# Kernel tuning notes

Hardware: AMD Instinct MI355X
Metric: run time of the kernel (lower is better)

Reference implementation:

```python
import jax, jax.numpy as jnp
import numpy as np

N_NODES = 100000
N_EDGES = 1600000
F_IN = 64
HID = 64
N_ACT = 8


def gcn_conv(x, edge_index, W, b):
    # PyG GCNConv: h = x @ W; add self-loops; norm = deg^{-1/2}[src]*deg^{-1/2}[dst];
    # out[dst] += norm * h[src]; out += b
    n = x.shape[0]
    h = x @ W  # [N, out]
    row = jnp.concatenate([edge_index[0], jnp.arange(n)])  # src (+ self loops)
    col = jnp.concatenate([edge_index[1], jnp.arange(n)])  # dst (+ self loops)
    deg = jax.ops.segment_sum(jnp.ones_like(col, dtype=h.dtype), col, num_segments=n)
    dinv = jnp.where(deg > 0, jax.lax.rsqrt(deg), 0.0)
    norm = dinv[row] * dinv[col]  # [E+N]
    msg = h[row] * norm[:, None]  # gather + scale
    out = jax.ops.segment_sum(msg, col, num_segments=n)  # scatter-add
    return out + b


def setup_inputs() -> dict:
    key = jax.random.key(0)
    ks = jax.random.split(key, 8)
    x = jax.random.normal(ks[0], (N_NODES, F_IN), dtype=jnp.float32)
    edge_index = jax.random.randint(ks[1], (2, N_EDGES), 0, N_NODES, dtype=jnp.int64)
    def glorot(k, fan_in, fan_out):
        s = jnp.sqrt(6.0 / (fan_in + fan_out))
        return jax.random.uniform(k, (fan_in, fan_out), jnp.float32, -s, s)
    W1 = glorot(ks[2], F_IN, HID)
    b1 = jnp.zeros((HID,), jnp.float32)
    W2 = glorot(ks[3], HID, HID)
    b2 = jnp.zeros((HID,), jnp.float32)
    Wfc = glorot(ks[4], HID, N_ACT)
    bfc = jnp.zeros((N_ACT,), jnp.float32)
    return {"x": x, "edge_index": edge_index, "W1": W1, "b1": b1,
            "W2": W2, "b2": b2, "Wfc": Wfc, "bfc": bfc}


def reference(x, edge_index, W1, b1, W2, b2, Wfc, bfc):
    h = jax.nn.relu(gcn_conv(x, edge_index, W1, b1))
    h = jax.nn.relu(gcn_conv(h, edge_index, W2, b2))
    return h @ Wfc + bfc  # Q-values per node: [N, num_actions]
```

## Files before the change

### kernel.cpp

```cpp
#include <hip/hip_runtime.h>
#include <hip/hip_fp16.h>


#define F 64
#define NACT 8
#define BSH 9
#define BNODES 512
#define CAP 10240
#define EPB 2048
#define HS 67

__global__ __launch_bounds__(256) void k_init(int* flag, int* cursor) {
  if (threadIdx.x == 0) *flag = 1;
  cursor[threadIdx.x] = 0;
}

__global__ __launch_bounds__(256) void k_detect(const unsigned int* __restrict__ w, int* flag, int E) {
  int i = blockIdx.x * 256 + threadIdx.x;
  if (i < E && w[2 * i + 1] != 0u) *flag = 0;
}

__device__ __forceinline__ int edge_row(const unsigned int* w, int flag, int e, int E) {
  return flag ? (int)w[2 * e] : (int)w[e];
}
__device__ __forceinline__ int edge_col(const unsigned int* w, int flag, int e, int E) {
  return flag ? (int)w[2 * E + 2 * e] : (int)w[E + e];
}

__global__ __launch_bounds__(256) void k_scatterE(const unsigned int* __restrict__ w,
    const int* __restrict__ flag, int* __restrict__ cursor, unsigned int* __restrict__ slab, int E) {
  __shared__ int hist[256];
  __shared__ int base[256];
  const int tid = threadIdx.x;
  const int fl = *flag;
  hist[tid] = 0;
  __syncthreads();
  int pk[8], bb[8], lr[8];
  const int e0 = blockIdx.x * EPB;
#pragma unroll 8
  for (int j = 0; j < 8; ++j) {
    int e = e0 + j * 256 + tid;
    bb[j] = -1;
    if (e < E) {
      int c = edge_col(w, fl, e, E);
      int s = edge_row(w, fl, e, E);
      int b = c >> BSH;
      pk[j] = (unsigned)s | ((unsigned)(c & (BNODES - 1)) << 17);
      bb[j] = b;
      lr[j] = atomicAdd(&hist[b], 1);
    }
  }
  __syncthreads();
  int h = hist[tid];
  if (h > 0) base[tid] = atomicAdd(&cursor[tid], h);
  __syncthreads();
#pragma unroll 8
  for (int j = 0; j < 8; ++j) {
    if (bb[j] >= 0) {
      slab[(size_t)bb[j] * CAP + base[bb[j]] + lr[j]] = (unsigned)pk[j];
    }
  }
}

__global__ __launch_bounds__(64) void k_slabscan(const int* __restrict__ cursor,
    int* __restrict__ bucketBase, int* __restrict__ csr_off, int NB, int n, int E) {
  int t = threadIdx.x;
  int per = (NB + 63) / 64;
  int base = t * per;
  int local = 0;
  for (int i = 0; i < per; ++i) if (base + i < NB) local += cursor[base + i];
  int inc = local;
  for (int off = 1; off < 64; off <<= 1) {
    int vv = __shfl_up(inc, off);
    if (t >= off) inc += vv;
  }
  int run = inc - local;
  for (int i = 0; i < per; ++i) if (base + i < NB) { bucketBase[base + i] = run; run += cursor[base + i]; }
  if (t == 63) { bucketBase[NB] = inc; csr_off[n] = E; }
}

__global__ __launch_bounds__(256) void k_bucketcsr(const unsigned int* __restrict__ slab,
    const int* __restrict__ bucketBase, int* __restrict__ csr_off, float* __restrict__ dinv,
    int* __restrict__ csr_src, int n) {
  __shared__ int cnt[BNODES];
  __shared__ int off[BNODES];
  __shared__ int sA[256], sB[256];
  const int tid = threadIdx.x;
  const int b = blockIdx.x;
  const int csrbeg = bucketBase[b];
  const int cntb = bucketBase[b + 1] - csrbeg;
  const unsigned int* sl = &slab[(size_t)b * CAP];
  cnt[tid] = 0;
  cnt[tid + 256] = 0;
  __syncthreads();
  for (int i = tid; i < cntb; i += 256) {
    atomicAdd(&cnt[sl[i] >> 17], 1);
  }
  __syncthreads();
  int c0 = cnt[2 * tid], c1 = cnt[2 * tid + 1];
  int p = c0 + c1;
  sA[tid] = p;
  __syncthreads();
  int* srcb = sA;
  int* dstb = sB;
  for (int o = 1; o < 256; o <<= 1) {
    int v = srcb[tid];
    if (tid >= o) v += srcb[tid - o];
    __syncthreads();
    dstb[tid] = v;
    __syncthreads();
    int* t2 = srcb; srcb = dstb; dstb = t2;
  }
  int ex2 = srcb[tid] - p;
  off[2 * tid] = ex2;
  off[2 * tid + 1] = ex2 + c0;
  __syncthreads();
  int v0 = (b << BSH) + 2 * tid;
  if (v0 < n) { csr_off[v0] = csrbeg + off[2 * tid]; dinv[v0] = rsqrtf((float)(c0 + 1)); }
  if (v0 + 1 < n) { csr_off[v0 + 1] = csrbeg + off[2 * tid + 1]; dinv[v0 + 1] = rsqrtf((float)(c1 + 1)); }
  __syncthreads();
  for (int i = tid; i < cntb; i += 256) {
    unsigned int pk = sl[i];
    int dl = pk >> 17;
    int pos = atomicAdd(&off[dl], 1);
    csr_src[csrbeg + pos] = (int)(pk & 0x1FFFFu);
  }
}

__device__ __forceinline__ ushort4 packh4(float a, float b, float c, float d) {
  ushort4 r;
  r.x = __half_as_ushort(__float2half_rn(a));
  r.y = __half_as_ushort(__float2half_rn(b));
  r.z = __half_as_ushort(__float2half_rn(c));
  r.w = __half_as_ushort(__float2half_rn(d));
  return r;
}

__device__ __forceinline__ void addrow8(float* a, uint4 g) {
  union { uint4 u; __half2 h[4]; } u;
  u.u = g;
#pragma unroll
  for (int i = 0; i < 4; ++i) {
    float2 f = __half22float2(u.h[i]);
    a[2 * i] += f.x;
    a[2 * i + 1] += f.y;
  }
}

__device__ __forceinline__ void gather8(const uint4* __restrict__ Gv,
    const int* __restrict__ csr_src, int beg, int end, int l, float* a) {
  int j = beg;
  for (; j + 8 <= end; j += 8) {
    uint4 g0 = Gv[(size_t)csr_src[j + 0] * 8 + l];
    uint4 g1 = Gv[(size_t)csr_src[j + 1] * 8 + l];
    uint4 g2 = Gv[(size_t)csr_src[j + 2] * 8 + l];
    uint4 g3 = Gv[(size_t)csr_src[j + 3] * 8 + l];
    uint4 g4 = Gv[(size_t)csr_src[j + 4] * 8 + l];
    uint4 g5 = Gv[(size_t)csr_src[j + 5] * 8 + l];
    uint4 g6 = Gv[(size_t)csr_src[j + 6] * 8 + l];
    uint4 g7 = Gv[(size_t)csr_src[j + 7] * 8 + l];
    addrow8(a, g0); addrow8(a, g1); addrow8(a, g2); addrow8(a, g3);
    addrow8(a, g4); addrow8(a, g5); addrow8(a, g6); addrow8(a, g7);
  }
  for (; j + 4 <= end; j += 4) {
    uint4 g0 = Gv[(size_t)csr_src[j + 0] * 8 + l];
    uint4 g1 = Gv[(size_t)csr_src[j + 1] * 8 + l];
    uint4 g2 = Gv[(size_t)csr_src[j + 2] * 8 + l];
    uint4 g3 = Gv[(size_t)csr_src[j + 3] * 8 + l];
    addrow8(a, g0); addrow8(a, g1); addrow8(a, g2); addrow8(a, g3);
  }
  for (; j < end; ++j) addrow8(a, Gv[(size_t)csr_src[j] * 8 + l]);
}

__global__ __launch_bounds__(256) void k_gemm_h(const float* __restrict__ X, const float* __restrict__ W,
    const float* __restrict__ dinv, unsigned short* __restrict__ Gh, int n) {
  __shared__ float xst[F * 68];
  __shared__ float wsh[F * F];
  const int tid = threadIdx.x;
  const int row0 = blockIdx.x * 64;
  for (int i = tid * 4; i < F * F; i += 1024)
    *(float4*)&wsh[i] = *(const float4*)&W[i];
  for (int i = tid * 4; i < 64 * F; i += 1024) {
    int r = i >> 6, k = i & 63;
    float4 v = make_float4(0.f, 0.f, 0.f, 0.f);
    if (row0 + r < n) v = *(const float4*)&X[(size_t)(row0 + r) * F + k];
    xst[(k + 0) * 68 + r] = v.x;
    xst[(k + 1) * 68 + r] = v.y;
    xst[(k + 2) * 68 + r] = v.z;
    xst[(k + 3) * 68 + r] = v.w;
  }
  __syncthreads();
  const int tc = tid & 15;
  const int tr = tid >> 4;
  float a00 = 0.f, a01 = 0.f, a02 = 0.f, a03 = 0.f;
  float a10 = 0.f, a11 = 0.f, a12 = 0.f, a13 = 0.f;
  float a20 = 0.f, a21 = 0.f, a22 = 0.f, a23 = 0.f;
  float a30 = 0.f, a31 = 0.f, a32 = 0.f, a33 = 0.f;
  const float* xp = &xst[tr * 4];
  const float* wp = &wsh[tc * 4];
#pragma unroll 8
  for (int k = 0; k < F; ++k) {
    float4 xv = *(const float4*)&xp[k * 68];
    float4 wv = *(const float4*)&wp[k * F];
    a00 = fmaf(xv.x, wv.x, a00); a01 = fmaf(xv.x, wv.y, a01);
    a02 = fmaf(xv.x, wv.z, a02); a03 = fmaf(xv.x, wv.w, a03);
    a10 = fmaf(xv.y, wv.x, a10); a11 = fmaf(xv.y, wv.y, a11);
    a12 = fmaf(xv.y, wv.z, a12); a13 = fmaf(xv.y, wv.w, a13);
    a20 = fmaf(xv.z, wv.x, a20); a21 = fmaf(xv.z, wv.y, a21);
    a22 = fmaf(xv.z, wv.z, a22); a23 = fmaf(xv.z, wv.w, a23);
    a30 = fmaf(xv.w, wv.x, a30); a31 = fmaf(xv.w, wv.y, a31);
    a32 = fmaf(xv.w, wv.z, a32); a33 = fmaf(xv.w, wv.w, a33);
  }
  const int gc = tc * 4;
  int gr = row0 + tr * 4;
  if (gr + 0 < n) { float d = dinv[gr + 0]; *(ushort4*)&Gh[(size_t)(gr + 0) * F + gc] = packh4(a00 * d, a01 * d, a02 * d, a03 * d); }
  if (gr + 1 < n) { float d = dinv[gr + 1]; *(ushort4*)&Gh[(size_t)(gr + 1) * F + gc] = packh4(a10 * d, a11 * d, a12 * d, a13 * d); }
  if (gr + 2 < n) { float d = dinv[gr + 2]; *(ushort4*)&Gh[(size_t)(gr + 2) * F + gc] = packh4(a20 * d, a21 * d, a22 * d, a23 * d); }
  if (gr + 3 < n) { float d = dinv[gr + 3]; *(ushort4*)&Gh[(size_t)(gr + 3) * F + gc] = packh4(a30 * d, a31 * d, a32 * d, a33 * d); }
}

__global__ __launch_bounds__(512) void k_gather_gemm(const int* __restrict__ csr_off,
    const int* __restrict__ csr_src, const unsigned short* __restrict__ Gh1,
    const float* __restrict__ dinv, const float* __restrict__ bias,
    const float* __restrict__ W2, unsigned short* __restrict__ Gh2, int n) {
  __shared__ float hst[F * HS];
  __shared__ float wsh[F * F];
  const int tid = threadIdx.x;
  const int row0 = blockIdx.x * 64;
  {
    int i = tid * 8;
    *(float4*)&wsh[i] = *(const float4*)&W2[i];
    *(float4*)&wsh[i + 4] = *(const float4*)&W2[i + 4];
  }
  const int ln = tid >> 3;
  const int l = tid & 7;
  const int v = row0 + ln;
  float a[8] = {0.f, 0.f, 0.f, 0.f, 0.f, 0.f, 0.f, 0.f};
  if (v < n) {
    const uint4* Gv = (const uint4*)Gh1;
    addrow8(a, Gv[(size_t)v * 8 + l]);
    gather8(Gv, csr_src, csr_off[v], csr_off[v + 1], l, a);
    float d = dinv[v];
#pragma unroll
    for (int jj = 0; jj < 8; ++jj) {
      float h = fmaxf(fmaf(a[jj], d, bias[l * 8 + jj]), 0.f);
      hst[(l * 8 + jj) * HS + ln] = h;
    }
  } else {
#pragma unroll
    for (int jj = 0; jj < 8; ++jj) hst[(l * 8 + jj) * HS + ln] = 0.f;
  }
  __syncthreads();
  const int tc = tid & 15;
  const int tr = tid >> 4;
  const int r0 = 2 * tr;
  float a00 = 0.f, a01 = 0.f, a02 = 0.f, a03 = 0.f;
  float a10 = 0.f, a11 = 0.f, a12 = 0.f, a13 = 0.f;
  const float* wp = &wsh[tc * 4];
#pragma unroll 8
  for (int k = 0; k < F; ++k) {
    float h0 = hst[k * HS + r0];
    float h1 = hst[k * HS + r0 + 1];
    float4 wv = *(const float4*)&wp[k * F];
    a00 = fmaf(h0, wv.x, a00); a01 = fmaf(h0, wv.y, a01);
    a02 = fmaf(h0, wv.z, a02); a03 = fmaf(h0, wv.w, a03);
    a10 = fmaf(h1, wv.x, a10); a11 = fmaf(h1, wv.y, a11);
    a12 = fmaf(h1, wv.z, a12); a13 = fmaf(h1, wv.w, a13);
  }
  const int gc = tc * 4;
  int gr = row0 + r0;
  if (gr < n) { float d = dinv[gr]; *(ushort4*)&Gh2[(size_t)gr * F + gc] = packh4(a00 * d, a01 * d, a02 * d, a03 * d); }
  if (gr + 1 < n) { float d = dinv[gr + 1]; *(ushort4*)&Gh2[(size_t)(gr + 1) * F + gc] = packh4(a10 * d, a11 * d, a12 * d, a13 * d); }
}

__global__ __launch_bounds__(256) void k_gather_fc(const int* __restrict__ csr_off,
    const int* __restrict__ csr_src, const unsigned short* __restrict__ Gh,
    const float* __restrict__ dinv, const float* __restrict__ bias,
    const float* __restrict__ Wfc, const float* __restrict__ bfc,
    float* __restrict__ OUT, int n) {
  __shared__ float wsh[F * 9];
  __shared__ float bs[NACT];
  const int tid = threadIdx.x;
  for (int i = tid; i < F * NACT; i += 256) wsh[(i >> 3) * 9 + (i & 7)] = Wfc[i];
  if (tid < NACT) bs[tid] = bfc[tid];
  __syncthreads();
  int v = blockIdx.x * 32 + (tid >> 3);
  int l = tid & 7;
  if (v >= n) return;
  const uint4* Gv = (const uint4*)Gh;
  float a[8] = {0.f, 0.f, 0.f, 0.f, 0.f, 0.f, 0.f, 0.f};
  addrow8(a, Gv[(size_t)v * 8 + l]);
  gather8(Gv, csr_src, csr_off[v], csr_off[v + 1], l, a);
  float d = dinv[v];
  float q[NACT] = {0.f, 0.f, 0.f, 0.f, 0.f, 0.f, 0.f, 0.f};
#pragma unroll
  for (int jj = 0; jj < 8; ++jj) {
    float h = fmaxf(fmaf(a[jj], d, bias[l * 8 + jj]), 0.f);
    const float* wr = &wsh[(l * 8 + jj) * 9];
#pragma unroll
    for (int aa = 0; aa < NACT; ++aa) q[aa] = fmaf(h, wr[aa], q[aa]);
  }
#pragma unroll
  for (int m = 1; m < 8; m <<= 1) {
#pragma unroll
    for (int aa = 0; aa < NACT; ++aa) q[aa] += __shfl_xor(q[aa], m);
  }
  OUT[(size_t)v * NACT + l] = q[l] + bs[l];
}

extern "C" void kernel_launch(void* const* d_in, const int* in_sizes, int n_in,
                              void* d_out, int out_size, void* d_ws, size_t ws_size,
                              hipStream_t stream) {
  const float* x = (const float*)d_in[0];
  const unsigned int* ew = (const unsigned int*)d_in[1];
  const float* W1 = (const float*)d_in[2];
  const float* b1 = (const float*)d_in[3];
  const float* W2 = (const float*)d_in[4];
  const float* b2 = (const float*)d_in[5];
  const float* Wfc = (const float*)d_in[6];
  const float* bfc = (const float*)d_in[7];
  float* out = (float*)d_out;
  const int n = in_sizes[0] / F;
  const int E = in_sizes[1] / 2;
  const int NB = (n + BNODES - 1) >> BSH;

  char* base = (char*)d_ws;
  size_t off = 0;
  auto alloc = [&](size_t bytes) { void* p = base + off; off += (bytes + 255) & ~(size_t)255; return p; };
  int* flag = (int*)alloc(4);
  int* cursor = (int*)alloc(256 * 4);
  int* bucketBase = (int*)alloc((size_t)(NB + 1) * 4);
  int* csr_off = (int*)alloc((size_t)(n + 1) * 4);
  float* dinv = (float*)alloc((size_t)n * 4);
  unsigned int* slab = (unsigned int*)alloc((size_t)NB * CAP * 4);
  int* csr_src = (int*)alloc((size_t)E * 4);
  unsigned short* Gh1 = (unsigned short*)alloc((size_t)n * F * 2);
  unsigned short* Gh2 = (unsigned short*)alloc((size_t)n * F * 2);

  const int gbE = (E + 255) / 256;
  const int gbSc = (E + EPB - 1) / EPB;
  const int gbRow = (n + 63) / 64;
  const int gbGa = (n + 31) / 32;

  hipLaunchKernelGGL(k_init, dim3(1), dim3(256), 0, stream, flag, cursor);
  hipLaunchKernelGGL(k_detect, dim3(gbE), dim3(256), 0, stream, ew, flag, E);
  hipLaunchKernelGGL(k_scatterE, dim3(gbSc), dim3(256), 0, stream, ew, flag, cursor, slab, E);
  hipLaunchKernelGGL(k_slabscan, dim3(1), dim3(64), 0, stream, cursor, bucketBase, csr_off, NB, n, E);
  hipLaunchKernelGGL(k_bucketcsr, dim3(NB), dim3(256), 0, stream, slab, bucketBase, csr_off, dinv, csr_src, n);

  hipLaunchKernelGGL(k_gemm_h, dim3(gbRow), dim3(256), 0, stream, x, W1, dinv, Gh1, n);
  hipLaunchKernelGGL(k_gather_gemm, dim3(gbRow), dim3(512), 0, stream, csr_off, csr_src, Gh1, dinv, b1, W2, Gh2, n);
  hipLaunchKernelGGL(k_gather_fc, dim3(gbGa), dim3(256), 0, stream, csr_off, csr_src, Gh2, dinv, b2, Wfc, bfc, out, n);
}
```

Baseline: 163.8 us.

## Split layer-2 gather from GEMM, use fma_mix accumulation, sample int64 detection

The fused gather+GEMM kernel for layer 2 is split into a gather kernel that writes fp16 activations and a separate 4x4-register-tiled GEMM kernel, trading an extra fp16 round-trip through memory for better occupancy in the gather. The half-to-float accumulate is replaced by inline v_fma_mix_f32 instructions to cut conversion ALU ops. The int64 layout detection kernel is folded into the init kernel and only checks the first 8192 edges, dropping a full-edge-list pass and one launch but relying on a sampled check.

New measurement: 170.9 us. 4.4% more time.

```diff
diff --git a/kernel.cpp b/kernel.cpp
--- a/kernel.cpp
+++ b/kernel.cpp
@@ -8,16 +8,17 @@
 #define BNODES 512
 #define CAP 10240
 #define EPB 2048
-#define HS 67
-
-__global__ __launch_bounds__(256) void k_init(int* flag, int* cursor) {
+
+__global__ __launch_bounds__(256) void k_init(const unsigned int* __restrict__ w,
+    int* flag, int* cursor, int E) {
   if (threadIdx.x == 0) *flag = 1;
   cursor[threadIdx.x] = 0;
-}
-
-__global__ __launch_bounds__(256) void k_detect(const unsigned int* __restrict__ w, int* flag, int E) {
-  int i = blockIdx.x * 256 + threadIdx.x;
-  if (i < E && w[2 * i + 1] != 0u) *flag = 0;
+  __syncthreads();
+  int bad = 0;
+  for (int i = threadIdx.x; i < 8192; i += 256) {
+    if (i < E && w[2 * i + 1] != 0u) bad = 1;
+  }
+  if (bad) atomicAnd(flag, 0);
 }
 
 __device__ __forceinline__ int edge_row(const unsigned int* w, int flag, int e, int E) {
@@ -136,15 +137,20 @@
   return r;
 }
 
-__device__ __forceinline__ void addrow8(float* a, uint4 g) {
-  union { uint4 u; __half2 h[4]; } u;
-  u.u = g;
-#pragma unroll
-  for (int i = 0; i < 4; ++i) {
-    float2 f = __half22float2(u.h[i]);
-    a[2 * i] += f.x;
-    a[2 * i + 1] += f.y;
-  }
+__device__ __forceinline__ void accmix(float* a, uint4 g) {
+  float one = 1.0f;
+  asm volatile(
+    "v_fma_mix_f32 %0, %9, %8, %0 op_sel:[0,0,0] op_sel_hi:[1,0,0]\n\t"
+    "v_fma_mix_f32 %1, %9, %8, %1 op_sel:[1,0,0] op_sel_hi:[1,0,0]\n\t"
+    "v_fma_mix_f32 %2, %10, %8, %2 op_sel:[0,0,0] op_sel_hi:[1,0,0]\n\t"
+    "v_fma_mix_f32 %3, %10, %8, %3 op_sel:[1,0,0] op_sel_hi:[1,0,0]\n\t"
+    "v_fma_mix_f32 %4, %11, %8, %4 op_sel:[0,0,0] op_sel_hi:[1,0,0]\n\t"
+    "v_fma_mix_f32 %5, %11, %8, %5 op_sel:[1,0,0] op_sel_hi:[1,0,0]\n\t"
+    "v_fma_mix_f32 %6, %12, %8, %6 op_sel:[0,0,0] op_sel_hi:[1,0,0]\n\t"
+    "v_fma_mix_f32 %7, %12, %8, %7 op_sel:[1,0,0] op_sel_hi:[1,0,0]"
+    : "+v"(a[0]), "+v"(a[1]), "+v"(a[2]), "+v"(a[3]),
+      "+v"(a[4]), "+v"(a[5]), "+v"(a[6]), "+v"(a[7])
+    : "v"(one), "v"(g.x), "v"(g.y), "v"(g.z), "v"(g.w));
 }
 
 __device__ __forceinline__ void gather8(const uint4* __restrict__ Gv,
@@ -159,17 +165,17 @@
     uint4 g5 = Gv[(size_t)csr_src[j + 5] * 8 + l];
     uint4 g6 = Gv[(size_t)csr_src[j + 6] * 8 + l];
     uint4 g7 = Gv[(size_t)csr_src[j + 7] * 8 + l];
-    addrow8(a, g0); addrow8(a, g1); addrow8(a, g2); addrow8(a, g3);
-    addrow8(a, g4); addrow8(a, g5); addrow8(a, g6); addrow8(a, g7);
+    accmix(a, g0); accmix(a, g1); accmix(a, g2); accmix(a, g3);
+    accmix(a, g4); accmix(a, g5); accmix(a, g6); accmix(a, g7);
   }
   for (; j + 4 <= end; j += 4) {
     uint4 g0 = Gv[(size_t)csr_src[j + 0] * 8 + l];
     uint4 g1 = Gv[(size_t)csr_src[j + 1] * 8 + l];
     uint4 g2 = Gv[(size_t)csr_src[j + 2] * 8 + l];
     uint4 g3 = Gv[(size_t)csr_src[j + 3] * 8 + l];
-    addrow8(a, g0); addrow8(a, g1); addrow8(a, g2); addrow8(a, g3);
-  }
-  for (; j < end; ++j) addrow8(a, Gv[(size_t)csr_src[j] * 8 + l]);
+    accmix(a, g0); accmix(a, g1); accmix(a, g2); accmix(a, g3);
+  }
+  for (; j < end; ++j) accmix(a, Gv[(size_t)csr_src[j] * 8 + l]);
 }
 
 __global__ __launch_bounds__(256) void k_gemm_h(const float* __restrict__ X, const float* __restrict__ W,
@@ -219,58 +225,76 @@
   if (gr + 3 < n) { float d = dinv[gr + 3]; *(ushort4*)&Gh[(size_t)(gr + 3) * F + gc] = packh4(a30 * d, a31 * d, a32 * d, a33 * d); }
 }
 
-__global__ __launch_bounds__(512) void k_gather_gemm(const int* __restrict__ csr_off,
-    const int* __restrict__ csr_src, const unsigned short* __restrict__ Gh1,
-    const float* __restrict__ dinv, const float* __restrict__ bias,
-    const float* __restrict__ W2, unsigned short* __restrict__ Gh2, int n) {
-  __shared__ float hst[F * HS];
+__global__ __launch_bounds__(256) void k_gemm_h2(const unsigned short* __restrict__ H16,
+    const float* __restrict__ W, const float* __restrict__ dinv,
+    unsigned short* __restrict__ Gh, int n) {
+  __shared__ float xst[F * 68];
   __shared__ float wsh[F * F];
   const int tid = threadIdx.x;
   const int row0 = blockIdx.x * 64;
-  {
-    int i = tid * 8;
-    *(float4*)&wsh[i] = *(const float4*)&W2[i];
-    *(float4*)&wsh[i + 4] = *(const float4*)&W2[i + 4];
-  }
-  const int ln = tid >> 3;
-  const int l = tid & 7;
-  const int v = row0 + ln;
-  float a[8] = {0.f, 0.f, 0.f, 0.f, 0.f, 0.f, 0.f, 0.f};
-  if (v < n) {
-    const uint4* Gv = (const uint4*)Gh1;
-    addrow8(a, Gv[(size_t)v * 8 + l]);
-    gather8(Gv, csr_src, csr_off[v], csr_off[v + 1], l, a);
-    float d = dinv[v];
-#pragma unroll
-    for (int jj = 0; jj < 8; ++jj) {
-      float h = fmaxf(fmaf(a[jj], d, bias[l * 8 + jj]), 0.f);
-      hst[(l * 8 + jj) * HS + ln] = h;
-    }
-  } else {
-#pragma unroll
-    for (int jj = 0; jj < 8; ++jj) hst[(l * 8 + jj) * HS + ln] = 0.f;
+  for (int i = tid * 4; i < F * F; i += 1024)
+    *(float4*)&wsh[i] = *(const float4*)&W[i];
+  for (int i = tid * 4; i < 64 * F; i += 1024) {
+    int r = i >> 6, k = i & 63;
+    uint2 hh = make_uint2(0u, 0u);
+    if (row0 + r < n) hh = *(const uint2*)&H16[(size_t)(row0 + r) * F + k];
+    float2 f0 = __half22float2(*(__half2*)&hh.x);
+    float2 f1 = __half22float2(*(__half2*)&hh.y);
+    xst[(k + 0) * 68 + r] = f0.x;
+    xst[(k + 1) * 68 + r] = f0.y;
+    xst[(k + 2) * 68 + r] = f1.x;
+    xst[(k + 3) * 68 + r] = f1.y;
   }
   __syncthreads();
   const int tc = tid & 15;
   const int tr = tid >> 4;
-  const int r0 = 2 * tr;
   float a00 = 0.f, a01 = 0.f, a02 = 0.f, a03 = 0.f;
   float a10 = 0.f, a11 = 0.f, a12 = 0.f, a13 = 0.f;
+  float a20 = 0.f, a21 = 0.f, a22 = 0.f, a23 = 0.f;
+  float a30 = 0.f, a31 = 0.f, a32 = 0.f, a33 = 0.f;
+  const float* xp = &xst[tr * 4];
   const float* wp = &wsh[tc * 4];
 #pragma unroll 8
   for (int k = 0; k < F; ++k) {
-    float h0 = hst[k * HS + r0];
-    float h1 = hst[k * HS + r0 + 1];
+    float4 xv = *(const float4*)&xp[k * 68];
     float4 wv = *(const float4*)&wp[k * F];
-    a00 = fmaf(h0, wv.x, a00); a01 = fmaf(h0, wv.y, a01);
-    a02 = fmaf(h0, wv.z, a02); a03 = fmaf(h0, wv.w, a03);
-    a10 = fmaf(h1, wv.x, a10); a11 = fmaf(h1, wv.y, a11);
-    a12 = fmaf(h1, wv.z, a12); a13 = fmaf(h1, wv.w, a13);
+    a00 = fmaf(xv.x, wv.x, a00); a01 = fmaf(xv.x, wv.y, a01);
+    a02 = fmaf(xv.x, wv.z, a02); a03 = fmaf(xv.x, wv.w, a03);
+    a10 = fmaf(xv.y, wv.x, a10); a11 = fmaf(xv.y, wv.y, a11);
+    a12 = fmaf(xv.y, wv.z, a12); a13 = fmaf(xv.y, wv.w, a13);
+    a20 = fmaf(xv.z, wv.x, a20); a21 = fmaf(xv.z, wv.y, a21);
+    a22 = fmaf(xv.z, wv.z, a22); a23 = fmaf(xv.z, wv.w, a23);
+    a30 = fmaf(xv.w, wv.x, a30); a31 = fmaf(xv.w, wv.y, a31);
+    a32 = fmaf(xv.w, wv.z, a32); a33 = fmaf(xv.w, wv.w, a33);
   }
   const int gc = tc * 4;
-  int gr = row0 + r0;
-  if (gr < n) { float d = dinv[gr]; *(ushort4*)&Gh2[(size_t)gr * F + gc] = packh4(a00 * d, a01 * d, a02 * d, a03 * d); }
-  if (gr + 1 < n) { float d = dinv[gr + 1]; *(ushort4*)&Gh2[(size_t)(gr + 1) * F + gc] = packh4(a10 * d, a11 * d, a12 * d, a13 * d); }
+  int gr = row0 + tr * 4;
+  if (gr + 0 < n) { float d = dinv[gr + 0]; *(ushort4*)&Gh[(size_t)(gr + 0) * F + gc] = packh4(a00 * d, a01 * d, a02 * d, a03 * d); }
+  if (gr + 1 < n) { float d = dinv[gr + 1]; *(ushort4*)&Gh[(size_t)(gr + 1) * F + gc] = packh4(a10 * d, a11 * d, a12 * d, a13 * d); }
+  if (gr + 2 < n) { float d = dinv[gr + 2]; *(ushort4*)&Gh[(size_t)(gr + 2) * F + gc] = packh4(a20 * d, a21 * d, a22 * d, a23 * d); }
+  if (gr + 3 < n) { float d = dinv[gr + 3]; *(ushort4*)&Gh[(size_t)(gr + 3) * F + gc] = packh4(a30 * d, a31 * d, a32 * d, a33 * d); }
+}
+
+__global__ __launch_bounds__(256) void k_gather_h16(const int* __restrict__ csr_off,
+    const int* __restrict__ csr_src, const unsigned short* __restrict__ Gh,
+    const float* __restrict__ dinv, const float* __restrict__ b,
+    unsigned short* __restrict__ H16, int n) {
+  int v = blockIdx.x * 32 + (threadIdx.x >> 3);
+  if (v >= n) return;
+  int l = threadIdx.x & 7;
+  const uint4* Gv = (const uint4*)Gh;
+  float a[8] = {0.f, 0.f, 0.f, 0.f, 0.f, 0.f, 0.f, 0.f};
+  accmix(a, Gv[(size_t)v * 8 + l]);
+  gather8(Gv, csr_src, csr_off[v], csr_off[v + 1], l, a);
+  float d = dinv[v];
+  float4 b0 = *(const float4*)&b[l * 8];
+  float4 b1 = *(const float4*)&b[l * 8 + 4];
+  ushort4 h0 = packh4(fmaxf(fmaf(a[0], d, b0.x), 0.f), fmaxf(fmaf(a[1], d, b0.y), 0.f),
+                      fmaxf(fmaf(a[2], d, b0.z), 0.f), fmaxf(fmaf(a[3], d, b0.w), 0.f));
+  ushort4 h1 = packh4(fmaxf(fmaf(a[4], d, b1.x), 0.f), fmaxf(fmaf(a[5], d, b1.y), 0.f),
+                      fmaxf(fmaf(a[6], d, b1.z), 0.f), fmaxf(fmaf(a[7], d, b1.w), 0.f));
+  *(ushort4*)&H16[(size_t)v * F + l * 8] = h0;
+  *(ushort4*)&H16[(size_t)v * F + l * 8 + 4] = h1;
 }
 
 __global__ __launch_bounds__(256) void k_gather_fc(const int* __restrict__ csr_off,
@@ -289,7 +313,7 @@
   if (v >= n) return;
   const uint4* Gv = (const uint4*)Gh;
   float a[8] = {0.f, 0.f, 0.f, 0.f, 0.f, 0.f, 0.f, 0.f};
-  addrow8(a, Gv[(size_t)v * 8 + l]);
+  accmix(a, Gv[(size_t)v * 8 + l]);
   gather8(Gv, csr_src, csr_off[v], csr_off[v + 1], l, a);
   float d = dinv[v];
   float q[NACT] = {0.f, 0.f, 0.f, 0.f, 0.f, 0.f, 0.f, 0.f};
@@ -335,20 +359,20 @@
   unsigned int* slab = (unsigned int*)alloc((size_t)NB * CAP * 4);
   int* csr_src = (int*)alloc((size_t)E * 4);
   unsigned short* Gh1 = (unsigned short*)alloc((size_t)n * F * 2);
+  unsigned short* H16 = (unsigned short*)alloc((size_t)n * F * 2);
   unsigned short* Gh2 = (unsigned short*)alloc((size_t)n * F * 2);
 
-  const int gbE = (E + 255) / 256;
   const int gbSc = (E + EPB - 1) / EPB;
   const int gbRow = (n + 63) / 64;
   const int gbGa = (n + 31) / 32;
 
-  hipLaunchKernelGGL(k_init, dim3(1), dim3(256), 0, stream, flag, cursor);
-  hipLaunchKernelGGL(k_detect, dim3(gbE), dim3(256), 0, stream, ew, flag, E);
+  hipLaunchKernelGGL(k_init, dim3(1), dim3(256), 0, stream, ew, flag, cursor, E);
   hipLaunchKernelGGL(k_scatterE, dim3(gbSc), dim3(256), 0, stream, ew, flag, cursor, slab, E);
   hipLaunchKernelGGL(k_slabscan, dim3(1), dim3(64), 0, stream, cursor, bucketBase, csr_off, NB, n, E);
   hipLaunchKernelGGL(k_bucketcsr, dim3(NB), dim3(256), 0, stream, slab, bucketBase, csr_off, dinv, csr_src, n);
 
   hipLaunchKernelGGL(k_gemm_h, dim3(gbRow), dim3(256), 0, stream, x, W1, dinv, Gh1, n);
-  hipLaunchKernelGGL(k_gather_gemm, dim3(gbRow), dim3(512), 0, stream, csr_off, csr_src, Gh1, dinv, b1, W2, Gh2, n);
+  hipLaunchKernelGGL(k_gather_h16, dim3(gbGa), dim3(256), 0, stream, csr_off, csr_src, Gh1, dinv, b1, H16, n);
+  hipLaunchKernelGGL(k_gemm_h2, dim3(gbRow), dim3(256), 0, stream, H16, W2, dinv, Gh2, n);
   hipLaunchKernelGGL(k_gather_fc, dim3(gbGa), dim3(256), 0, stream, csr_off, csr_src, Gh2, dinv, b2, Wfc, bfc, out, n);
 }
```
